# Optimization experiments

Hardware: AMD Instinct MI355X
Metric: run time of the kernel (lower is better)

Reference implementation:

```python
import jax, jax.numpy as jnp
import numpy as np

LN_EPS = 1e-5


def _ssm_scan(x_ssm, A, Bm, C, reverse):
    # x_ssm: [B, L, d_inner]; A, Bm, C: [d_inner, d_state]
    Bb, L, di = x_ssm.shape
    ds = Bm.shape[1]

    def step(h, x_t):
        # h: [B, d_inner, d_state], x_t: [B, d_inner]
        h = jnp.clip(h * A[None] + x_t[:, :, None] * Bm[None], -10.0, 10.0)
        y = jnp.einsum('bid,id->bi', h, C)
        return h, y

    h0 = jnp.zeros((Bb, di, ds), x_ssm.dtype)
    _, ys = jax.lax.scan(step, h0, jnp.swapaxes(x_ssm, 0, 1), reverse=reverse)
    return jnp.swapaxes(ys, 0, 1)  # [B, L, d_inner], time-ordered


def setup_inputs() -> dict:
    key = jax.random.key(0)
    ks = jax.random.split(key, 6)
    B, L, D = 4, 2048, 1024
    d_state, expand = 16, 2
    d_inner = D * expand
    x = jax.random.normal(ks[0], (B, L, D), jnp.float32)
    # xavier-ish scaled params
    in_proj_w = jax.random.normal(ks[1], (d_inner * 2, D), jnp.float32) * np.float32(1.0 / np.sqrt(D))
    A_log = jax.random.normal(ks[2], (d_inner, d_state), jnp.float32)
    B_mat = jax.random.normal(ks[3], (d_inner, d_state), jnp.float32) * np.float32(1.0 / np.sqrt(d_state))
    C_mat = jnp.full((d_inner, d_state), 0.01, jnp.float32)
    out_proj_w = jax.random.normal(ks[4], (D, d_inner), jnp.float32) * np.float32(1.0 / np.sqrt(d_inner))
    ln_w = jnp.ones((D,), jnp.float32)
    ln_b = jnp.zeros((D,), jnp.float32)
    return {"x": x, "in_proj_w": in_proj_w, "A_log": A_log, "B_mat": B_mat,
            "C_mat": C_mat, "out_proj_w": out_proj_w, "ln_w": ln_w, "ln_b": ln_b}


def reference(x, in_proj_w, A_log, B_mat, C_mat, out_proj_w, ln_w, ln_b):
    # LayerNorm
    mu = jnp.mean(x, axis=-1, keepdims=True)
    var = jnp.mean((x - mu) ** 2, axis=-1, keepdims=True)
    xn = (x - mu) * jax.lax.rsqrt(var + LN_EPS) * ln_w + ln_b
    # in_proj (no bias), split into ssm stream and gate
    x_proj = jnp.einsum('bld,ed->ble', xn, in_proj_w)  # [B, L, 2*d_inner]
    x_ssm, gate = jnp.split(x_proj, 2, axis=-1)
    # A = -clamp(exp(A_log), -10, -0.01)  (saturates to 0.01, kept faithfully)
    A = -jnp.clip(jnp.exp(A_log), -10.0, -0.01)
    out_f = _ssm_scan(x_ssm, A, B_mat, C_mat, reverse=False)
    out_b = _ssm_scan(x_ssm, A, B_mat, C_mat, reverse=True)
    out = (out_f + out_b) * 0.5 * jax.nn.silu(gate)
    return jnp.einsum('bli,di->bld', out, out_proj_w)
```

## Files before the change

kernel.cpp:

```cpp
#include <hip/hip_runtime.h>

typedef __attribute__((ext_vector_type(8))) _Float16 f16x8;
typedef __attribute__((ext_vector_type(4))) float f32x4;

#define GLOBAL_AS __attribute__((address_space(1)))
#define LDS_AS __attribute__((address_space(3)))

static constexpr int Bb = 4, LL = 2048, DD = 1024, DI = 2048, DS = 16;
static constexpr int MROWS = Bb * LL;
static constexpr int N1 = 2 * DI;
static constexpr int K1 = DD;
static constexpr int N2 = DD;
static constexpr int K2 = DI;

__device__ __forceinline__ unsigned short f2h(float f) {
  _Float16 h = (_Float16)f;
  union { _Float16 h; unsigned short u; } c; c.h = h;
  return c.u;
}
__device__ __forceinline__ float h2f(unsigned short u) {
  union { unsigned short u; _Float16 h; } c; c.u = u;
  return (float)c.h;
}

__global__ __launch_bounds__(256) void ln_half_kernel(
    const float* __restrict__ x, const float* __restrict__ lnw,
    const float* __restrict__ lnb, unsigned short* __restrict__ A1) {
  const int r = blockIdx.x;
  const int tid = threadIdx.x;
  const float4 v = reinterpret_cast<const float4*>(x + (size_t)r * DD)[tid];
  float s = v.x + v.y + v.z + v.w;
#pragma unroll
  for (int off = 32; off >= 1; off >>= 1) s += __shfl_xor(s, off, 64);
  __shared__ float red[8];
  const int wid = tid >> 6;
  if ((tid & 63) == 0) red[wid] = s;
  __syncthreads();
  const float mu = (red[0] + red[1] + red[2] + red[3]) * (1.0f / DD);
  const float dx = v.x - mu, dy = v.y - mu, dz = v.z - mu, dw = v.w - mu;
  float ss = dx * dx + dy * dy + dz * dz + dw * dw;
#pragma unroll
  for (int off = 32; off >= 1; off >>= 1) ss += __shfl_xor(ss, off, 64);
  if ((tid & 63) == 0) red[4 + wid] = ss;
  __syncthreads();
  const float var = (red[4] + red[5] + red[6] + red[7]) * (1.0f / DD);
  const float rs = rsqrtf(var + 1e-5f);
  const float4 w4 = reinterpret_cast<const float4*>(lnw)[tid];
  const float4 b4 = reinterpret_cast<const float4*>(lnb)[tid];
  ushort4 h4;
  h4.x = f2h(dx * rs * w4.x + b4.x);
  h4.y = f2h(dy * rs * w4.y + b4.y);
  h4.z = f2h(dz * rs * w4.z + b4.z);
  h4.w = f2h(dw * rs * w4.w + b4.w);
  *reinterpret_cast<ushort4*>(&A1[(size_t)r * DD + tid * 4]) = h4;
}

__global__ __launch_bounds__(256) void f32_to_f16_kernel(
    const float* __restrict__ W, unsigned short* __restrict__ O) {
  const int gid = blockIdx.x * 256 + threadIdx.x;
  const float4 w = reinterpret_cast<const float4*>(W)[gid];
  ushort4 h4;
  h4.x = f2h(w.x); h4.y = f2h(w.y); h4.z = f2h(w.z); h4.w = f2h(w.w);
  reinterpret_cast<ushort4*>(O)[gid] = h4;
}

__global__ __launch_bounds__(512, 2) void gemm_bt_256(
    const unsigned short* __restrict__ A, const unsigned short* __restrict__ B,
    unsigned short* __restrict__ C, int M, int N, int K) {
  __shared__ unsigned short sm[2][2][256 * 64];
  const int tid = threadIdx.x;
  const int wid = tid >> 6;
  const int lane = tid & 63;
  const int wm = wid >> 2;
  const int wn = wid & 3;
  const int mt = M >> 8;
  const int cpx = gridDim.x >> 3;
  const int bid = blockIdx.x;
  const int sw = (bid & 7) * cpx + (bid >> 3);
  const int bm = sw % mt;
  const int bn = sw / mt;
  const size_t arow0 = (size_t)bm * 256;
  const size_t brow0 = (size_t)bn * 256;

  const unsigned short* gA[4];
  const unsigned short* gB[4];
#pragma unroll
  for (int j = 0; j < 4; ++j) {
    const int idx = j * 512 + tid;
    const int prow = idx >> 3;
    const int scol = ((idx & 7) ^ (prow & 7)) << 3;
    gA[j] = A + (arow0 + prow) * (size_t)K + scol;
    gB[j] = B + (brow0 + prow) * (size_t)K + scol;
  }
  auto stageA = [&](int buf) {
#pragma unroll
    for (int j = 0; j < 4; ++j) {
      __builtin_amdgcn_global_load_lds((const GLOBAL_AS void*)gA[j],
          (LDS_AS void*)&sm[buf][0][(j * 512 + (wid << 6)) * 8], 16, 0, 0);
      gA[j] += 64;
    }
  };
  auto stageB = [&](int buf) {
#pragma unroll
    for (int j = 0; j < 4; ++j) {
      __builtin_amdgcn_global_load_lds((const GLOBAL_AS void*)gB[j],
          (LDS_AS void*)&sm[buf][1][(j * 512 + (wid << 6)) * 8], 16, 0, 0);
      gB[j] += 64;
    }
  };

  const int q = lane >> 4;
  const int l7 = lane & 7;
  const int fr = lane & 15;
  int swz[2];
  swz[0] = (q << 3) ^ (l7 << 3);
  swz[1] = (32 + (q << 3)) ^ (l7 << 3);

  int arows[8], brows[4];
#pragma unroll
  for (int mf = 0; mf < 8; ++mf) arows[mf] = ((wm << 7) + mf * 16 + fr) * 64;
#pragma unroll
  for (int nf = 0; nf < 4; ++nf) brows[nf] = ((wn << 6) + nf * 16 + fr) * 64;

  f32x4 acc[8][4] = {};

  const int NTK = K >> 6;
  stageA(0);
  stageB(0);
  asm volatile("s_waitcnt vmcnt(0)" ::: "memory");
  __builtin_amdgcn_s_barrier();

  for (int t = 0; t < NTK; ++t) {
    const int cur = t & 1, nxt = cur ^ 1;
    const bool more = (t + 1 < NTK);
    f16x8 aF[4][2], bL[2][2], bH[2][2];
#pragma unroll
    for (int mf = 0; mf < 4; ++mf)
#pragma unroll
      for (int ks = 0; ks < 2; ++ks)
        aF[mf][ks] = *reinterpret_cast<const f16x8*>(&sm[cur][0][arows[mf] + swz[ks]]);
#pragma unroll
    for (int nf = 0; nf < 2; ++nf)
#pragma unroll
      for (int ks = 0; ks < 2; ++ks)
        bL[nf][ks] = *reinterpret_cast<const f16x8*>(&sm[cur][1][brows[nf] + swz[ks]]);
    if (more) stageA(nxt);
    __builtin_amdgcn_s_barrier();
    asm volatile("s_waitcnt lgkmcnt(0)" ::: "memory");
    __builtin_amdgcn_sched_barrier(0);
    __builtin_amdgcn_s_setprio(1);
#pragma unroll
    for (int mf = 0; mf < 4; ++mf)
#pragma unroll
      for (int nf = 0; nf < 2; ++nf)
#pragma unroll
        for (int ks = 0; ks < 2; ++ks)
          acc[mf][nf] = __builtin_amdgcn_mfma_f32_16x16x32_f16(
              aF[mf][ks], bL[nf][ks], acc[mf][nf], 0, 0, 0);
    __builtin_amdgcn_s_setprio(0);
    __builtin_amdgcn_s_barrier();
#pragma unroll
    for (int nf = 0; nf < 2; ++nf)
#pragma unroll
      for (int ks = 0; ks < 2; ++ks)
        bH[nf][ks] = *reinterpret_cast<const f16x8*>(&sm[cur][1][brows[2 + nf] + swz[ks]]);
    if (more) stageB(nxt);
    __builtin_amdgcn_s_barrier();
    asm volatile("s_waitcnt lgkmcnt(0)" ::: "memory");
    __builtin_amdgcn_sched_barrier(0);
    __builtin_amdgcn_s_setprio(1);
#pragma unroll
    for (int mf = 0; mf < 4; ++mf)
#pragma unroll
      for (int nf = 0; nf < 2; ++nf)
#pragma unroll
        for (int ks = 0; ks < 2; ++ks)
          acc[mf][2 + nf] = __builtin_amdgcn_mfma_f32_16x16x32_f16(
              aF[mf][ks], bH[nf][ks], acc[mf][2 + nf], 0, 0, 0);
    __builtin_amdgcn_s_setprio(0);
    __builtin_amdgcn_s_barrier();
#pragma unroll
    for (int mf = 0; mf < 4; ++mf)
#pragma unroll
      for (int ks = 0; ks < 2; ++ks)
        aF[mf][ks] = *reinterpret_cast<const f16x8*>(&sm[cur][0][arows[4 + mf] + swz[ks]]);
    __builtin_amdgcn_s_barrier();
    asm volatile("s_waitcnt lgkmcnt(0)" ::: "memory");
    __builtin_amdgcn_sched_barrier(0);
    __builtin_amdgcn_s_setprio(1);
#pragma unroll
    for (int mf = 0; mf < 4; ++mf)
#pragma unroll
      for (int nf = 0; nf < 2; ++nf)
#pragma unroll
        for (int ks = 0; ks < 2; ++ks)
          acc[4 + mf][2 + nf] = __builtin_amdgcn_mfma_f32_16x16x32_f16(
              aF[mf][ks], bH[nf][ks], acc[4 + mf][2 + nf], 0, 0, 0);
    __builtin_amdgcn_s_setprio(0);
    __builtin_amdgcn_s_barrier();
    __builtin_amdgcn_s_setprio(1);
#pragma unroll
    for (int mf = 0; mf < 4; ++mf)
#pragma unroll
      for (int nf = 0; nf < 2; ++nf)
#pragma unroll
        for (int ks = 0; ks < 2; ++ks)
          acc[4 + mf][nf] = __builtin_amdgcn_mfma_f32_16x16x32_f16(
              aF[mf][ks], bL[nf][ks], acc[4 + mf][nf], 0, 0, 0);
    __builtin_amdgcn_s_setprio(0);
    if (more) asm volatile("s_waitcnt vmcnt(0)" ::: "memory");
    __builtin_amdgcn_s_barrier();
  }

  const int fcol = lane & 15;
  const int frow4 = (lane >> 4) << 2;
#pragma unroll
  for (int mf = 0; mf < 8; ++mf)
#pragma unroll
    for (int nf = 0; nf < 4; ++nf) {
      const size_t row0 = arow0 + (wm << 7) + mf * 16 + frow4;
      const size_t col = brow0 + (wn << 6) + nf * 16 + fcol;
#pragma unroll
      for (int j = 0; j < 4; ++j)
        C[(row0 + j) * (size_t)N + col] = f2h(acc[mf][nf][j]);
    }
}

__global__ __launch_bounds__(512, 2) void gemm_bt_256n128(
    const unsigned short* __restrict__ A, const unsigned short* __restrict__ B,
    float* __restrict__ C, int M, int N, int K) {
  __shared__ unsigned short sm[2][24576];
  const int tid = threadIdx.x;
  const int wid = tid >> 6;
  const int lane = tid & 63;
  const int wm = wid >> 2;
  const int wn = wid & 3;
  const int mt = M >> 8;
  const int cpx = gridDim.x >> 3;
  const int bid = blockIdx.x;
  const int sw = (bid & 7) * cpx + (bid >> 3);
  const int bm = sw % mt;
  const int bn = sw / mt;
  const size_t arow0 = (size_t)bm * 256;
  const size_t brow0 = (size_t)bn * 128;

  const unsigned short* gA[4];
  const unsigned short* gB[2];
#pragma unroll
  for (int j = 0; j < 4; ++j) {
    const int idx = j * 512 + tid;
    const int prow = idx >> 3;
    const int scol = ((idx & 7) ^ (prow & 7)) << 3;
    gA[j] = A + (arow0 + prow) * (size_t)K + scol;
  }
#pragma unroll
  for (int j = 0; j < 2; ++j) {
    const int idx = j * 512 + tid;
    const int prow = idx >> 3;
    const int scol = ((idx & 7) ^ (prow & 7)) << 3;
    gB[j] = B + (brow0 + prow) * (size_t)K + scol;
  }
  auto stageA = [&](int buf) {
#pragma unroll
    for (int j = 0; j < 4; ++j) {
      __builtin_amdgcn_global_load_lds((const GLOBAL_AS void*)gA[j],
          (LDS_AS void*)&sm[buf][(j * 512 + (wid << 6)) * 8], 16, 0, 0);
      gA[j] += 64;
    }
  };
  auto stageB = [&](int buf) {
#pragma unroll
    for (int j = 0; j < 2; ++j) {
      __builtin_amdgcn_global_load_lds((const GLOBAL_AS void*)gB[j],
          (LDS_AS void*)&sm[buf][16384 + (j * 512 + (wid << 6)) * 8], 16, 0, 0);
      gB[j] += 64;
    }
  };

  const int q = lane >> 4;
  const int l7 = lane & 7;
  const int fr = lane & 15;
  int swz[2];
  swz[0] = (q << 3) ^ (l7 << 3);
  swz[1] = (32 + (q << 3)) ^ (l7 << 3);

  int arows[8], brows[2];
#pragma unroll
  for (int mf = 0; mf < 8; ++mf) arows[mf] = ((wm << 7) + mf * 16 + fr) * 64;
#pragma unroll
  for (int nf = 0; nf < 2; ++nf) brows[nf] = 16384 + ((wn << 5) + nf * 16 + fr) * 64;

  f32x4 acc[8][2] = {};

  const int NTK = K >> 6;
  stageA(0);
  stageB(0);
  asm volatile("s_waitcnt vmcnt(0)" ::: "memory");
  __builtin_amdgcn_s_barrier();

  for (int t = 0; t < NTK; ++t) {
    const int cur = t & 1, nxt = cur ^ 1;
    const bool more = (t + 1 < NTK);
    f16x8 aF[4][2], bL[2], bH[2];
#pragma unroll
    for (int mf = 0; mf < 4; ++mf)
#pragma unroll
      for (int ks = 0; ks < 2; ++ks)
        aF[mf][ks] = *reinterpret_cast<const f16x8*>(&sm[cur][arows[mf] + swz[ks]]);
#pragma unroll
    for (int ks = 0; ks < 2; ++ks)
      bL[ks] = *reinterpret_cast<const f16x8*>(&sm[cur][brows[0] + swz[ks]]);
    if (more) stageA(nxt);
    __builtin_amdgcn_s_barrier();
    asm volatile("s_waitcnt lgkmcnt(0)" ::: "memory");
    __builtin_amdgcn_sched_barrier(0);
    __builtin_amdgcn_s_setprio(1);
#pragma unroll
    for (int mf = 0; mf < 4; ++mf)
#pragma unroll
      for (int ks = 0; ks < 2; ++ks)
        acc[mf][0] = __builtin_amdgcn_mfma_f32_16x16x32_f16(
            aF[mf][ks], bL[ks], acc[mf][0], 0, 0, 0);
    __builtin_amdgcn_s_setprio(0);
    __builtin_amdgcn_s_barrier();
#pragma unroll
    for (int ks = 0; ks < 2; ++ks)
      bH[ks] = *reinterpret_cast<const f16x8*>(&sm[cur][brows[1] + swz[ks]]);
    if (more) stageB(nxt);
    __builtin_amdgcn_s_barrier();
    asm volatile("s_waitcnt lgkmcnt(0)" ::: "memory");
    __builtin_amdgcn_sched_barrier(0);
    __builtin_amdgcn_s_setprio(1);
#pragma unroll
    for (int mf = 0; mf < 4; ++mf)
#pragma unroll
      for (int ks = 0; ks < 2; ++ks)
        acc[mf][1] = __builtin_amdgcn_mfma_f32_16x16x32_f16(
            aF[mf][ks], bH[ks], acc[mf][1], 0, 0, 0);
    __builtin_amdgcn_s_setprio(0);
    __builtin_amdgcn_s_barrier();
#pragma unroll
    for (int mf = 0; mf < 4; ++mf)
#pragma unroll
      for (int ks = 0; ks < 2; ++ks)
        aF[mf][ks] = *reinterpret_cast<const f16x8*>(&sm[cur][arows[4 + mf] + swz[ks]]);
    __builtin_amdgcn_s_barrier();
    asm volatile("s_waitcnt lgkmcnt(0)" ::: "memory");
    __builtin_amdgcn_sched_barrier(0);
    __builtin_amdgcn_s_setprio(1);
#pragma unroll
    for (int mf = 0; mf < 4; ++mf)
#pragma unroll
      for (int ks = 0; ks < 2; ++ks)
        acc[4 + mf][1] = __builtin_amdgcn_mfma_f32_16x16x32_f16(
            aF[mf][ks], bH[ks], acc[4 + mf][1], 0, 0, 0);
    __builtin_amdgcn_s_setprio(0);
    __builtin_amdgcn_s_barrier();
    __builtin_amdgcn_s_setprio(1);
#pragma unroll
    for (int mf = 0; mf < 4; ++mf)
#pragma unroll
      for (int ks = 0; ks < 2; ++ks)
        acc[4 + mf][0] = __builtin_amdgcn_mfma_f32_16x16x32_f16(
            aF[mf][ks], bL[ks], acc[4 + mf][0], 0, 0, 0);
    __builtin_amdgcn_s_setprio(0);
    if (more) asm volatile("s_waitcnt vmcnt(0)" ::: "memory");
    __builtin_amdgcn_s_barrier();
  }

  const int fcol = lane & 15;
  const int frow4 = (lane >> 4) << 2;
#pragma unroll
  for (int mf = 0; mf < 8; ++mf)
#pragma unroll
    for (int nf = 0; nf < 2; ++nf) {
      const size_t row0 = arow0 + (wm << 7) + mf * 16 + frow4;
      const size_t col = brow0 + (wn << 5) + nf * 16 + fcol;
#pragma unroll
      for (int j = 0; j < 4; ++j)
        C[(row0 + j) * (size_t)N + col] = acc[mf][nf][j];
    }
}

__global__ __launch_bounds__(256) void scan_kernel(
    const unsigned short* __restrict__ xp, const float* __restrict__ Bm,
    const float* __restrict__ Cm, unsigned short* __restrict__ oss) {
  constexpr int T = 32, KH = 8;
  const int blk = blockIdx.x;
  const int igrp = blk & 7;
  const int c = (blk >> 3) & 63;
  const int b = blk >> 9;
  const int tid = threadIdx.x;
  const int i = igrp * 256 + tid;
  float d = 0.f;
  {
    const float4* bp = reinterpret_cast<const float4*>(Bm + (size_t)i * DS);
    const float4* cp = reinterpret_cast<const float4*>(Cm + (size_t)i * DS);
#pragma unroll
    for (int qv = 0; qv < 4; ++qv) {
      const float4 bv = bp[qv], cv = cp[qv];
      d += bv.x * cv.x + bv.y * cv.y + bv.z * cv.z + bv.w * cv.w;
    }
  }
  const float dh = 0.5f * d;
  const int t0 = c * T;
  const size_t rowbase = (size_t)b * LL;
  float yf[T];
  float g = 0.f;
  {
    const int hstart = (t0 >= KH) ? t0 - KH : 0;
    for (int t = hstart; t < t0; ++t)
      g = fmaf(0.01f, g, h2f(xp[(rowbase + t) * (size_t)N1 + i]));
#pragma unroll
    for (int j = 0; j < T; ++j) {
      g = fmaf(0.01f, g, h2f(xp[(rowbase + t0 + j) * (size_t)N1 + i]));
      yf[j] = g;
    }
  }
  g = 0.f;
  {
    const int tend = (t0 + T - 1 + KH <= LL - 1) ? (t0 + T - 1 + KH) : (LL - 1);
    for (int t = tend; t >= t0 + T; --t)
      g = fmaf(0.01f, g, h2f(xp[(rowbase + t) * (size_t)N1 + i]));
#pragma unroll
    for (int j = T - 1; j >= 0; --j) {
      const size_t row = rowbase + t0 + j;
      g = fmaf(0.01f, g, h2f(xp[row * (size_t)N1 + i]));
      const float gt = h2f(xp[row * (size_t)N1 + DI + i]);
      const float sg = gt / (1.f + expf(-gt));
      const float o = (yf[j] + g) * dh * sg;
      oss[row * (size_t)DI + i] = f2h(o);
    }
  }
}

extern "C" void kernel_launch(void* const* d_in, const int* in_sizes, int n_in,
                              void* d_out, int out_size, void* d_ws, size_t ws_size,
                              hipStream_t stream) {
  (void)in_sizes; (void)n_in; (void)out_size; (void)ws_size;
  const float* x          = (const float*)d_in[0];
  const float* in_proj_w  = (const float*)d_in[1];
  const float* B_mat      = (const float*)d_in[3];
  const float* C_mat      = (const float*)d_in[4];
  const float* out_proj_w = (const float*)d_in[5];
  const float* ln_w       = (const float*)d_in[6];
  const float* ln_b       = (const float*)d_in[7];
  float* out = (float*)d_out;

  char* ws = (char*)d_ws;
  unsigned short* A1  = (unsigned short*)ws; ws += (size_t)MROWS * K1 * 2;
  unsigned short* B1  = (unsigned short*)ws; ws += (size_t)N1 * K1 * 2;
  unsigned short* B2  = (unsigned short*)ws; ws += (size_t)N2 * K2 * 2;
  unsigned short* OSS = (unsigned short*)ws; ws += (size_t)MROWS * DI * 2;
  unsigned short* XP  = (unsigned short*)ws; ws += (size_t)MROWS * N1 * 2;

  f32_to_f16_kernel<<<dim3((N1 * K1 / 4) / 256), dim3(256), 0, stream>>>(in_proj_w, B1);
  f32_to_f16_kernel<<<dim3((N2 * K2 / 4) / 256), dim3(256), 0, stream>>>(out_proj_w, B2);
  ln_half_kernel<<<dim3(MROWS), dim3(256), 0, stream>>>(x, ln_w, ln_b, A1);
  gemm_bt_256<<<dim3((MROWS / 256) * (N1 / 256)), dim3(512), 0, stream>>>(A1, B1, XP, MROWS, N1, K1);
  scan_kernel<<<dim3(2048), dim3(256), 0, stream>>>(XP, B_mat, C_mat, OSS);
  gemm_bt_256n128<<<dim3((MROWS / 256) * (N2 / 128)), dim3(512), 0, stream>>>(OSS, B2, out, MROWS, N2, K2);
}
```

Before: 191.0 us.

## Replace hand-interleaved ping-pong GEMM schedule with simple prefetch-then-compute loop

Both GEMM kernels drop the fine-grained schedule, which interleaved LDS reads, global staging, barriers, s_setprio and sched_barrier across four MFMA quadrants. Each k-tile now issues the global staging for the next tile, loads all A/B fragments from LDS, runs every MFMA, then synchronises once with __syncthreads. The aim is to cut barrier count and let the compiler schedule freely, at the cost of more live fragment registers and less explicit overlap between memory and MFMA work.

```diff
diff --git a/kernel.cpp b/kernel.cpp
--- a/kernel.cpp
+++ b/kernel.cpp
@@ -127,89 +127,31 @@
   const int NTK = K >> 6;
   stageA(0);
   stageB(0);
-  asm volatile("s_waitcnt vmcnt(0)" ::: "memory");
-  __builtin_amdgcn_s_barrier();
+  __syncthreads();
 
   for (int t = 0; t < NTK; ++t) {
     const int cur = t & 1, nxt = cur ^ 1;
-    const bool more = (t + 1 < NTK);
-    f16x8 aF[4][2], bL[2][2], bH[2][2];
-#pragma unroll
-    for (int mf = 0; mf < 4; ++mf)
+    if (t + 1 < NTK) { stageA(nxt); stageB(nxt); }
+    f16x8 af[8][2], bf[4][2];
+#pragma unroll
+    for (int mf = 0; mf < 8; ++mf)
 #pragma unroll
       for (int ks = 0; ks < 2; ++ks)
-        aF[mf][ks] = *reinterpret_cast<const f16x8*>(&sm[cur][0][arows[mf] + swz[ks]]);
-#pragma unroll
-    for (int nf = 0; nf < 2; ++nf)
+        af[mf][ks] = *reinterpret_cast<const f16x8*>(&sm[cur][0][arows[mf] + swz[ks]]);
+#pragma unroll
+    for (int nf = 0; nf < 4; ++nf)
 #pragma unroll
       for (int ks = 0; ks < 2; ++ks)
-        bL[nf][ks] = *reinterpret_cast<const f16x8*>(&sm[cur][1][brows[nf] + swz[ks]]);
-    if (more) stageA(nxt);
-    __builtin_amdgcn_s_barrier();
-    asm volatile("s_waitcnt lgkmcnt(0)" ::: "memory");
-    __builtin_amdgcn_sched_barrier(0);
-    __builtin_amdgcn_s_setprio(1);
-#pragma unroll
-    for (int mf = 0; mf < 4; ++mf)
-#pragma unroll
-      for (int nf = 0; nf < 2; ++nf)
-#pragma unroll
-        for (int ks = 0; ks < 2; ++ks)
+        bf[nf][ks] = *reinterpret_cast<const f16x8*>(&sm[cur][1][brows[nf] + swz[ks]]);
+#pragma unroll
+    for (int ks = 0; ks < 2; ++ks)
+#pragma unroll
+      for (int mf = 0; mf < 8; ++mf)
+#pragma unroll
+        for (int nf = 0; nf < 4; ++nf)
           acc[mf][nf] = __builtin_amdgcn_mfma_f32_16x16x32_f16(
-              aF[mf][ks], bL[nf][ks], acc[mf][nf], 0, 0, 0);
-    __builtin_amdgcn_s_setprio(0);
-    __builtin_amdgcn_s_barrier();
-#pragma unroll
-    for (int nf = 0; nf < 2; ++nf)
-#pragma unroll
-      for (int ks = 0; ks < 2; ++ks)
-        bH[nf][ks] = *reinterpret_cast<const f16x8*>(&sm[cur][1][brows[2 + nf] + swz[ks]]);
-    if (more) stageB(nxt);
-    __builtin_amdgcn_s_barrier();
-    asm volatile("s_waitcnt lgkmcnt(0)" ::: "memory");
-    __builtin_amdgcn_sched_barrier(0);
-    __builtin_amdgcn_s_setprio(1);
-#pragma unroll
-    for (int mf = 0; mf < 4; ++mf)
-#pragma unroll
-      for (int nf = 0; nf < 2; ++nf)
-#pragma unroll
-        for (int ks = 0; ks < 2; ++ks)
-          acc[mf][2 + nf] = __builtin_amdgcn_mfma_f32_16x16x32_f16(
-              aF[mf][ks], bH[nf][ks], acc[mf][2 + nf], 0, 0, 0);
-    __builtin_amdgcn_s_setprio(0);
-    __builtin_amdgcn_s_barrier();
-#pragma unroll
-    for (int mf = 0; mf < 4; ++mf)
-#pragma unroll
-      for (int ks = 0; ks < 2; ++ks)
-        aF[mf][ks] = *reinterpret_cast<const f16x8*>(&sm[cur][0][arows[4 + mf] + swz[ks]]);
-    __builtin_amdgcn_s_barrier();
-    asm volatile("s_waitcnt lgkmcnt(0)" ::: "memory");
-    __builtin_amdgcn_sched_barrier(0);
-    __builtin_amdgcn_s_setprio(1);
-#pragma unroll
-    for (int mf = 0; mf < 4; ++mf)
-#pragma unroll
-      for (int nf = 0; nf < 2; ++nf)
-#pragma unroll
-        for (int ks = 0; ks < 2; ++ks)
-          acc[4 + mf][2 + nf] = __builtin_amdgcn_mfma_f32_16x16x32_f16(
-              aF[mf][ks], bH[nf][ks], acc[4 + mf][2 + nf], 0, 0, 0);
-    __builtin_amdgcn_s_setprio(0);
-    __builtin_amdgcn_s_barrier();
-    __builtin_amdgcn_s_setprio(1);
-#pragma unroll
-    for (int mf = 0; mf < 4; ++mf)
-#pragma unroll
-      for (int nf = 0; nf < 2; ++nf)
-#pragma unroll
-        for (int ks = 0; ks < 2; ++ks)
-          acc[4 + mf][nf] = __builtin_amdgcn_mfma_f32_16x16x32_f16(
-              aF[mf][ks], bL[nf][ks], acc[4 + mf][nf], 0, 0, 0);
-    __builtin_amdgcn_s_setprio(0);
-    if (more) asm volatile("s_waitcnt vmcnt(0)" ::: "memory");
-    __builtin_amdgcn_s_barrier();
+              af[mf][ks], bf[nf][ks], acc[mf][nf], 0, 0, 0);
+    __syncthreads();
   }
 
   const int fcol = lane & 15;
@@ -295,77 +237,31 @@
   const int NTK = K >> 6;
   stageA(0);
   stageB(0);
-  asm volatile("s_waitcnt vmcnt(0)" ::: "memory");
-  __builtin_amdgcn_s_barrier();
+  __syncthreads();
 
   for (int t = 0; t < NTK; ++t) {
     const int cur = t & 1, nxt = cur ^ 1;
-    const bool more = (t + 1 < NTK);
-    f16x8 aF[4][2], bL[2], bH[2];
-#pragma unroll
-    for (int mf = 0; mf < 4; ++mf)
+    if (t + 1 < NTK) { stageA(nxt); stageB(nxt); }
+    f16x8 af[8][2], bf[2][2];
+#pragma unroll
+    for (int mf = 0; mf < 8; ++mf)
 #pragma unroll
       for (int ks = 0; ks < 2; ++ks)
-        aF[mf][ks] = *reinterpret_cast<const f16x8*>(&sm[cur][arows[mf] + swz[ks]]);
+        af[mf][ks] = *reinterpret_cast<const f16x8*>(&sm[cur][arows[mf] + swz[ks]]);
+#pragma unroll
+    for (int nf = 0; nf < 2; ++nf)
+#pragma unroll
+      for (int ks = 0; ks < 2; ++ks)
+        bf[nf][ks] = *reinterpret_cast<const f16x8*>(&sm[cur][brows[nf] + swz[ks]]);
 #pragma unroll
     for (int ks = 0; ks < 2; ++ks)
-      bL[ks] = *reinterpret_cast<const f16x8*>(&sm[cur][brows[0] + swz[ks]]);
-    if (more) stageA(nxt);
-    __builtin_amdgcn_s_barrier();
-    asm volatile("s_waitcnt lgkmcnt(0)" ::: "memory");
-    __builtin_amdgcn_sched_barrier(0);
-    __builtin_amdgcn_s_setprio(1);
-#pragma unroll
-    for (int mf = 0; mf < 4; ++mf)
-#pragma unroll
-      for (int ks = 0; ks < 2; ++ks)
-        acc[mf][0] = __builtin_amdgcn_mfma_f32_16x16x32_f16(
-            aF[mf][ks], bL[ks], acc[mf][0], 0, 0, 0);
-    __builtin_amdgcn_s_setprio(0);
-    __builtin_amdgcn_s_barrier();
-#pragma unroll
-    for (int ks = 0; ks < 2; ++ks)
-      bH[ks] = *reinterpret_cast<const f16x8*>(&sm[cur][brows[1] + swz[ks]]);
-    if (more) stageB(nxt);
-    __builtin_amdgcn_s_barrier();
-    asm volatile("s_waitcnt lgkmcnt(0)" ::: "memory");
-    __builtin_amdgcn_sched_barrier(0);
-    __builtin_amdgcn_s_setprio(1);
-#pragma unroll
-    for (int mf = 0; mf < 4; ++mf)
-#pragma unroll
-      for (int ks = 0; ks < 2; ++ks)
-        acc[mf][1] = __builtin_amdgcn_mfma_f32_16x16x32_f16(
-            aF[mf][ks], bH[ks], acc[mf][1], 0, 0, 0);
-    __builtin_amdgcn_s_setprio(0);
-    __builtin_amdgcn_s_barrier();
-#pragma unroll
-    for (int mf = 0; mf < 4; ++mf)
-#pragma unroll
-      for (int ks = 0; ks < 2; ++ks)
-        aF[mf][ks] = *reinterpret_cast<const f16x8*>(&sm[cur][arows[4 + mf] + swz[ks]]);
-    __builtin_amdgcn_s_barrier();
-    asm volatile("s_waitcnt lgkmcnt(0)" ::: "memory");
-    __builtin_amdgcn_sched_barrier(0);
-    __builtin_amdgcn_s_setprio(1);
-#pragma unroll
-    for (int mf = 0; mf < 4; ++mf)
-#pragma unroll
-      for (int ks = 0; ks < 2; ++ks)
-        acc[4 + mf][1] = __builtin_amdgcn_mfma_f32_16x16x32_f16(
-            aF[mf][ks], bH[ks], acc[4 + mf][1], 0, 0, 0);
-    __builtin_amdgcn_s_setprio(0);
-    __builtin_amdgcn_s_barrier();
-    __builtin_amdgcn_s_setprio(1);
-#pragma unroll
-    for (int mf = 0; mf < 4; ++mf)
-#pragma unroll
-      for (int ks = 0; ks < 2; ++ks)
-        acc[4 + mf][0] = __builtin_amdgcn_mfma_f32_16x16x32_f16(
-            aF[mf][ks], bL[ks], acc[4 + mf][0], 0, 0, 0);
-    __builtin_amdgcn_s_setprio(0);
-    if (more) asm volatile("s_waitcnt vmcnt(0)" ::: "memory");
-    __builtin_amdgcn_s_barrier();
+#pragma unroll
+      for (int mf = 0; mf < 8; ++mf)
+#pragma unroll
+        for (int nf = 0; nf < 2; ++nf)
+          acc[mf][nf] = __builtin_amdgcn_mfma_f32_16x16x32_f16(
+              af[mf][ks], bf[nf][ks], acc[mf][nf], 0, 0, 0);
+    __syncthreads();
   }
 
   const int fcol = lane & 15;
```

Measured after the change: 181.9 us. 1.05x faster.
